# Kernel optimization log

Hardware: AMD Instinct MI355X
Metric: run time of the kernel (lower is better)

## Reference

```python
import math
import jax, jax.numpy as jnp
import numpy as np

B, S, D_MODEL, NUM_HEADS = 4, 2048, 1024, 16
D_N = D_MODEL // NUM_HEADS  # 64


def setup_inputs() -> dict:
    key = jax.random.key(0)
    ks = jax.random.split(key, 10)
    scale = 1.0 / math.sqrt(D_MODEL)
    return {
        "q": jax.random.normal(ks[0], (B, S, D_MODEL), dtype=jnp.float32),
        "k": jax.random.normal(ks[1], (B, S, D_MODEL), dtype=jnp.float32),
        "v": jax.random.normal(ks[2], (B, S, D_MODEL), dtype=jnp.float32),
        "mask": jax.random.uniform(ks[3], (B, S, S), dtype=jnp.float32),
        "w_q": jax.random.normal(ks[4], (D_N, D_MODEL), dtype=jnp.float32) * scale,
        "b_q": jnp.zeros((D_N,), dtype=jnp.float32),
        "w_k": jax.random.normal(ks[5], (D_N, D_MODEL), dtype=jnp.float32) * scale,
        "b_k": jnp.zeros((D_N,), dtype=jnp.float32),
        "w_v": jax.random.normal(ks[6], (D_N, D_MODEL), dtype=jnp.float32) * scale,
        "b_v": jnp.zeros((D_N,), dtype=jnp.float32),
    }


def reference(q, k, v, mask, w_q, b_q, w_k, b_k, w_v, b_v):
    # Linear projections d_model -> d_n (torch Linear: x @ W.T + b)
    qp = jnp.einsum("bsd,nd->bsn", q, w_q) + b_q  # [B,S,d_n]
    kp = jnp.einsum("bsd,nd->bsn", k, w_k) + b_k
    vp = jnp.einsum("bsd,nd->bsn", v, w_v) + b_v
    # Scaled dot-product scores with additive mask penalty
    scores = jnp.einsum("bqn,bkn->bqk", qp, kp) / math.sqrt(D_N) + mask * (-1e9)
    attn = jax.nn.softmax(scores, axis=-1)  # [B,S,S]
    return jnp.einsum("bqk,bkn->bqn", attn, vp)  # [B,S,d_n]
```

## Files before the change

### kernel.cpp

```cpp
#include <hip/hip_runtime.h>
#include <hip/hip_bf16.h>

#define BB 4
#define SS 2048
#define DM 1024
#define DN 64

typedef short short8 __attribute__((ext_vector_type(8)));
typedef float f32x4 __attribute__((ext_vector_type(4)));
typedef unsigned short ushort;

__device__ __forceinline__ ushort f2bf(float f) {
    union { float f; unsigned u; } v; v.f = f;
    unsigned r = v.u + 0x7fffu + ((v.u >> 16) & 1u);
    return (ushort)(r >> 16);
}
__device__ __forceinline__ float bf2f(ushort h) {
    union { unsigned u; float f; } v; v.u = ((unsigned)h) << 16; return v.f;
}

__global__ __launch_bounds__(256) void prep_w(
    const float* __restrict__ wq, const float* __restrict__ wk,
    const float* __restrict__ wv, ushort* __restrict__ w_bf)
{
    int i = blockIdx.x * 256 + threadIdx.x;
    int p = i >> 14;
    int j = (i & 16383) * 4;
    const float* src = (p == 0) ? wq : (p == 1) ? wk : wv;
    float4 f = *(const float4*)(src + j);
    ushort o[4] = { f2bf(f.x), f2bf(f.y), f2bf(f.z), f2bf(f.w) };
    *(unsigned long long*)(w_bf + p * 65536 + j) = *(unsigned long long*)o;
}

__global__ __launch_bounds__(256) void proj_kernel(
    const float* __restrict__ q, const float* __restrict__ k, const float* __restrict__ v,
    const ushort* __restrict__ w_bf,
    const float* __restrict__ bq, const float* __restrict__ bk, const float* __restrict__ bvp,
    ushort* __restrict__ qp, ushort* __restrict__ kp, ushort* __restrict__ vpT)
{
    __shared__ __align__(16) ushort A_lds[2][32][136];

    const int tid  = threadIdx.x;
    const int proj = blockIdx.y;
    const int m0   = blockIdx.x * 32;

    const float* x    = (proj == 0) ? q  : (proj == 1) ? k  : v;
    const ushort* wb  = w_bf + proj * 65536;
    const float* bias = (proj == 0) ? bq : (proj == 1) ? bk : bvp;

    const int wv   = tid >> 6;
    const int lane = tid & 63;
    const int l16  = lane & 15;
    const int quad = lane >> 4;
    const int rg   = wv & 1;
    const int nh   = wv >> 1;

    const int srow = tid >> 5;
    const int slc  = tid & 31;

    float4 pf[4];
    auto issue_loads = [&](int kb) {
#pragma unroll
        for (int r = 0; r < 4; r++)
            pf[r] = *(const float4*)&x[(size_t)(m0 + srow + r * 8) * DM + kb + slc * 4];
    };
    auto write_stage = [&](int buf) {
#pragma unroll
        for (int r = 0; r < 4; r++) {
            ushort t4[4] = { f2bf(pf[r].x), f2bf(pf[r].y), f2bf(pf[r].z), f2bf(pf[r].w) };
            *(unsigned long long*)&A_lds[buf][srow + r * 8][slc * 4] =
                *(unsigned long long*)t4;
        }
    };

    f32x4 acc[2];
    acc[0] = (f32x4){0.f, 0.f, 0.f, 0.f};
    acc[1] = (f32x4){0.f, 0.f, 0.f, 0.f};

    issue_loads(0);

#pragma unroll
    for (int s = 0; s < 8; s++) {
        const int buf = s & 1;
        write_stage(buf);
        if (s < 7) issue_loads((s + 1) * 128);
        __syncthreads();

        const int kb = s * 128;
#pragma unroll
        for (int kk = 0; kk < 128; kk += 32) {
            short8 a = *(const short8*)&A_lds[buf][rg * 16 + l16][kk + quad * 8];
#pragma unroll
            for (int tt = 0; tt < 2; tt++) {
                const int t = nh * 2 + tt;
                short8 b = *(const short8*)(wb + (size_t)(t * 16 + l16) * DM + kb + kk + quad * 8);
                acc[tt] = __builtin_amdgcn_mfma_f32_16x16x32_bf16(a, b, acc[tt], 0, 0, 0);
            }
        }
    }

#pragma unroll
    for (int tt = 0; tt < 2; tt++) {
        const int n = (nh * 2 + tt) * 16 + l16;
        float bb_ = bias[n];
#pragma unroll
        for (int r = 0; r < 4; r++) {
            int grow = m0 + rg * 16 + quad * 4 + r;
            ushort h = f2bf(acc[tt][r] + bb_);
            if (proj == 0)      qp[(size_t)grow * DN + n] = h;
            else if (proj == 1) kp[(size_t)grow * DN + n] = h;
            else {
                int bb = grow >> 11, ss = grow & 2047;
                vpT[((size_t)bb * DN + n) * SS + ss] = h;
            }
        }
    }
}

template<int KPS>
__global__ __launch_bounds__(256, 2) void flash_kernel(
    const float* __restrict__ mask,
    const ushort* __restrict__ qp,
    const ushort* __restrict__ kp,
    const ushort* __restrict__ vpT,
    ushort* __restrict__ part_O,
    float* __restrict__ part_ml)
{
    constexpr int NSLICE = SS / KPS;
    constexpr int NIT    = KPS / 64;

    __shared__ __align__(16) ushort p_lds[4][16][72];

    const int tid  = threadIdx.x;
    const int wv   = tid >> 6;
    const int lane = tid & 63;
    const int l16  = lane & 15;
    const int quad = lane >> 4;

    const int gw    = blockIdx.x * 4 + wv;
    const int qg    = gw & 127;
    const int rest  = gw >> 7;
    const int slice = rest % NSLICE;
    const int b     = rest / NSLICE;

    const ushort* qbase = qp + ((size_t)b * SS + qg * 16 + l16) * DN + quad * 8;
    short8 aq0 = *(const short8*)(qbase);
    short8 aq1 = *(const short8*)(qbase + 32);

    float m_r[4] = { -__builtin_inff(), -__builtin_inff(),
                     -__builtin_inff(), -__builtin_inff() };
    float l_r[4] = { 0.f, 0.f, 0.f, 0.f };
    f32x4 Oacc[4];
#pragma unroll
    for (int t = 0; t < 4; t++) Oacc[t] = (f32x4){0.f, 0.f, 0.f, 0.f};

    const size_t mrow0 = ((size_t)b * SS + qg * 16 + quad * 4) * SS;
    const int k_begin = slice * KPS;

    float  mk[2][4][4];
    short8 bk0[2][4], bk1[2][4];

    auto load_tile = [&](int buf, int k0) {
#pragma unroll
        for (int t = 0; t < 4; t++) {
            const ushort* kb_ = kp + ((size_t)b * SS + k0 + t * 16 + l16) * DN + quad * 8;
            bk0[buf][t] = *(const short8*)(kb_);
            bk1[buf][t] = *(const short8*)(kb_ + 32);
        }
#pragma unroll
        for (int t = 0; t < 4; t++)
#pragma unroll
            for (int r = 0; r < 4; r++)
                mk[buf][t][r] = mask[mrow0 + (size_t)r * SS + k0 + t * 16 + l16];
    };

    load_tile(0, k_begin);

#pragma unroll
    for (int it = 0; it < NIT; ++it) {
        const int cur = it & 1;
        const int k0  = k_begin + it * 64;

        if (it + 1 < NIT) load_tile(cur ^ 1, k0 + 64);

        short8 bv0[4], bv1[4];
#pragma unroll
        for (int tf = 0; tf < 4; tf++) {
            const ushort* vb_ = vpT + ((size_t)b * DN + tf * 16 + l16) * SS + k0 + quad * 8;
            bv0[tf] = *(const short8*)(vb_);
            bv1[tf] = *(const short8*)(vb_ + 32);
        }

        f32x4 sc[4];
#pragma unroll
        for (int t = 0; t < 4; t++) {
            f32x4 z = (f32x4){0.f, 0.f, 0.f, 0.f};
            z = __builtin_amdgcn_mfma_f32_16x16x32_bf16(aq0, bk0[cur][t], z, 0, 0, 0);
            z = __builtin_amdgcn_mfma_f32_16x16x32_bf16(aq1, bk1[cur][t], z, 0, 0, 0);
            sc[t] = z;
        }

#pragma unroll
        for (int r = 0; r < 4; r++) {
            float s[4];
            float tmax = -__builtin_inff();
#pragma unroll
            for (int t = 0; t < 4; t++) {
                s[t] = sc[t][r] * 0.125f - 1e9f * mk[cur][t][r];
                tmax = fmaxf(tmax, s[t]);
            }
#pragma unroll
            for (int off = 8; off >= 1; off >>= 1)
                tmax = fmaxf(tmax, __shfl_xor(tmax, off, 16));
            float mnew  = fmaxf(m_r[r], tmax);
            float alpha = __expf(m_r[r] - mnew);
            m_r[r] = mnew;
            float rs = 0.f;
#pragma unroll
            for (int t = 0; t < 4; t++) {
                float pv = __expf(s[t] - mnew);
                rs += pv;
                p_lds[wv][quad * 4 + r][t * 16 + l16] = f2bf(pv);
            }
#pragma unroll
            for (int off = 8; off >= 1; off >>= 1)
                rs += __shfl_xor(rs, off, 16);
            l_r[r] = l_r[r] * alpha + rs;
#pragma unroll
            for (int tf = 0; tf < 4; tf++)
                Oacc[tf][r] *= alpha;
        }

        short8 ap0 = *(const short8*)&p_lds[wv][l16][quad * 8];
        short8 ap1 = *(const short8*)&p_lds[wv][l16][32 + quad * 8];
#pragma unroll
        for (int tf = 0; tf < 4; tf++) {
            Oacc[tf] = __builtin_amdgcn_mfma_f32_16x16x32_bf16(ap0, bv0[tf], Oacc[tf], 0, 0, 0);
            Oacc[tf] = __builtin_amdgcn_mfma_f32_16x16x32_bf16(ap1, bv1[tf], Oacc[tf], 0, 0, 0);
        }
    }

    const int rowg = (b * SS + qg * 16) + quad * 4;
#pragma unroll
    for (int r = 0; r < 4; r++) {
        size_t row = (size_t)rowg + r;
        if (l16 == 0) {
            part_ml[((size_t)slice * (BB * SS) + row) * 2 + 0] = m_r[r];
            part_ml[((size_t)slice * (BB * SS) + row) * 2 + 1] = l_r[r];
        }
#pragma unroll
        for (int tf = 0; tf < 4; tf++)
            part_O[((size_t)slice * (BB * SS) + row) * DN + tf * 16 + l16] =
                f2bf(Oacc[tf][r]);
    }
}

__global__ __launch_bounds__(256) void combine_kernel(
    const ushort* __restrict__ part_O, const float* __restrict__ part_ml,
    float* __restrict__ out, int nslice)
{
    const int tid = threadIdx.x;
    const int row = blockIdx.x * 4 + (tid >> 6);
    const int f   = tid & 63;

    float ms[8], ls[8];
    float M = -__builtin_inff();
    for (int i = 0; i < nslice; i++) {
        ms[i] = part_ml[((size_t)i * (BB * SS) + row) * 2 + 0];
        ls[i] = part_ml[((size_t)i * (BB * SS) + row) * 2 + 1];
        M = fmaxf(M, ms[i]);
    }
    float L = 0.f, acc = 0.f;
    for (int i = 0; i < nslice; i++) {
        float e = __expf(ms[i] - M);
        L += e * ls[i];
        acc += e * bf2f(part_O[((size_t)i * (BB * SS) + row) * DN + f]);
    }
    out[(size_t)row * DN + f] = acc / L;
}

extern "C" void kernel_launch(void* const* d_in, const int* in_sizes, int n_in,
                              void* d_out, int out_size, void* d_ws, size_t ws_size,
                              hipStream_t stream) {
    const float* q    = (const float*)d_in[0];
    const float* k    = (const float*)d_in[1];
    const float* v    = (const float*)d_in[2];
    const float* mask = (const float*)d_in[3];
    const float* wq   = (const float*)d_in[4];
    const float* bq   = (const float*)d_in[5];
    const float* wk   = (const float*)d_in[6];
    const float* bk   = (const float*)d_in[7];
    const float* wv   = (const float*)d_in[8];
    const float* bv   = (const float*)d_in[9];
    float* out = (float*)d_out;

    char* p = (char*)d_ws;
    ushort* w_bf = (ushort*)p;   p += 3 * 65536 * sizeof(ushort);
    ushort* qp   = (ushort*)p;   p += (size_t)BB * SS * DN * 2;
    ushort* kp   = (ushort*)p;   p += (size_t)BB * SS * DN * 2;
    ushort* vpT  = (ushort*)p;   p += (size_t)BB * SS * DN * 2;
    size_t fixed = (size_t)(p - (char*)d_ws);

    int split = 8;
    for (;;) {
        size_t flash_bytes = (size_t)split * BB * SS * 2 * 4 + (size_t)split * BB * SS * DN * 2;
        if (split == 1 || fixed + flash_bytes <= ws_size) break;
        split >>= 1;
    }

    float*  part_ml = (float*)p;   p += (size_t)split * BB * SS * 2 * 4;
    ushort* part_O  = (ushort*)p;

    prep_w<<<192, 256, 0, stream>>>(wq, wk, wv, w_bf);
    proj_kernel<<<dim3(256, 3), 256, 0, stream>>>(q, k, v, w_bf, bq, bk, bv, qp, kp, vpT);
    switch (split) {
        case 8:  flash_kernel<256> <<<128 * 8, 256, 0, stream>>>(mask, qp, kp, vpT, part_O, part_ml); break;
        case 4:  flash_kernel<512> <<<128 * 4, 256, 0, stream>>>(mask, qp, kp, vpT, part_O, part_ml); break;
        case 2:  flash_kernel<1024><<<128 * 2, 256, 0, stream>>>(mask, qp, kp, vpT, part_O, part_ml); break;
        default: flash_kernel<2048><<<128 * 1, 256, 0, stream>>>(mask, qp, kp, vpT, part_O, part_ml); break;
    }
    combine_kernel<<<(BB * SS) / 4, 256, 0, stream>>>(part_O, part_ml, out, split);
}
```

Measured before the change: 226.9 us.

## Fuse weight conversion into projection, stage weights in LDS, MFMA row sums

Drops the separate prep_w launch. The projection kernel now converts fp32 weights to bf16 itself and stages them in LDS in 256-column chunks, while the activation rows are loaded straight into registers with a four-deep prefetch and converted per step. In the flash kernel the softmax is reorganised to batch the row-max shuffles across the four rows. The row sum is now computed with an extra MFMA against a ones vector instead of shuffle reductions. This removes one launch and the shuffle work, but every block re-reads and re-converts the weights, and the row sum now comes from bf16-rounded probabilities.

```diff
diff --git a/kernel.cpp b/kernel.cpp
--- a/kernel.cpp
+++ b/kernel.cpp
@@ -18,34 +18,26 @@
 __device__ __forceinline__ float bf2f(ushort h) {
     union { unsigned u; float f; } v; v.u = ((unsigned)h) << 16; return v.f;
 }
-
-__global__ __launch_bounds__(256) void prep_w(
-    const float* __restrict__ wq, const float* __restrict__ wk,
-    const float* __restrict__ wv, ushort* __restrict__ w_bf)
-{
-    int i = blockIdx.x * 256 + threadIdx.x;
-    int p = i >> 14;
-    int j = (i & 16383) * 4;
-    const float* src = (p == 0) ? wq : (p == 1) ? wk : wv;
-    float4 f = *(const float4*)(src + j);
-    ushort o[4] = { f2bf(f.x), f2bf(f.y), f2bf(f.z), f2bf(f.w) };
-    *(unsigned long long*)(w_bf + p * 65536 + j) = *(unsigned long long*)o;
-}
-
-__global__ __launch_bounds__(256) void proj_kernel(
+__device__ __forceinline__ short8 cvt8(float4 a, float4 b) {
+    ushort t[8] = { f2bf(a.x), f2bf(a.y), f2bf(a.z), f2bf(a.w),
+                    f2bf(b.x), f2bf(b.y), f2bf(b.z), f2bf(b.w) };
+    return *(short8*)t;
+}
+
+__global__ __launch_bounds__(256, 3) void proj_kernel(
     const float* __restrict__ q, const float* __restrict__ k, const float* __restrict__ v,
-    const ushort* __restrict__ w_bf,
+    const float* __restrict__ wq, const float* __restrict__ wk, const float* __restrict__ wvm,
     const float* __restrict__ bq, const float* __restrict__ bk, const float* __restrict__ bvp,
     ushort* __restrict__ qp, ushort* __restrict__ kp, ushort* __restrict__ vpT)
 {
-    __shared__ __align__(16) ushort A_lds[2][32][136];
+    __shared__ __align__(16) ushort B_lds[64][264];
 
     const int tid  = threadIdx.x;
     const int proj = blockIdx.y;
     const int m0   = blockIdx.x * 32;
 
     const float* x    = (proj == 0) ? q  : (proj == 1) ? k  : v;
-    const ushort* wb  = w_bf + proj * 65536;
+    const float* wm   = (proj == 0) ? wq : (proj == 1) ? wk : wvm;
     const float* bias = (proj == 0) ? bq : (proj == 1) ? bk : bvp;
 
     const int wv   = tid >> 6;
@@ -55,45 +47,44 @@
     const int rg   = wv & 1;
     const int nh   = wv >> 1;
 
-    const int srow = tid >> 5;
-    const int slc  = tid & 31;
-
-    float4 pf[4];
-    auto issue_loads = [&](int kb) {
-#pragma unroll
-        for (int r = 0; r < 4; r++)
-            pf[r] = *(const float4*)&x[(size_t)(m0 + srow + r * 8) * DM + kb + slc * 4];
-    };
-    auto write_stage = [&](int buf) {
-#pragma unroll
-        for (int r = 0; r < 4; r++) {
-            ushort t4[4] = { f2bf(pf[r].x), f2bf(pf[r].y), f2bf(pf[r].z), f2bf(pf[r].w) };
-            *(unsigned long long*)&A_lds[buf][srow + r * 8][slc * 4] =
-                *(unsigned long long*)t4;
-        }
-    };
+    const float* arow = x + (size_t)(m0 + rg * 16 + l16) * DM + quad * 8;
+
+    float4 apf[4][2];
+#pragma unroll
+    for (int s = 0; s < 4; s++) {
+        apf[s][0] = *(const float4*)(arow + s * 32);
+        apf[s][1] = *(const float4*)(arow + s * 32 + 4);
+    }
 
     f32x4 acc[2];
     acc[0] = (f32x4){0.f, 0.f, 0.f, 0.f};
     acc[1] = (f32x4){0.f, 0.f, 0.f, 0.f};
 
-    issue_loads(0);
-
-#pragma unroll
-    for (int s = 0; s < 8; s++) {
-        const int buf = s & 1;
-        write_stage(buf);
-        if (s < 7) issue_loads((s + 1) * 128);
+    for (int c = 0; c < 4; c++) {
         __syncthreads();
-
-        const int kb = s * 128;
-#pragma unroll
-        for (int kk = 0; kk < 128; kk += 32) {
-            short8 a = *(const short8*)&A_lds[buf][rg * 16 + l16][kk + quad * 8];
+#pragma unroll
+        for (int j = 0; j < 16; j++) {
+            int u   = tid + j * 256;
+            int row = u >> 6, c4 = u & 63;
+            float4 f = *(const float4*)(wm + (size_t)row * DM + c * 256 + c4 * 4);
+            ushort t4[4] = { f2bf(f.x), f2bf(f.y), f2bf(f.z), f2bf(f.w) };
+            *(unsigned long long*)&B_lds[row][c4 * 4] = *(unsigned long long*)t4;
+        }
+        __syncthreads();
+
+#pragma unroll
+        for (int kk = 0; kk < 8; kk++) {
+            const int step = c * 8 + kk;
+            const int ai   = step & 3;
+            short8 a = cvt8(apf[ai][0], apf[ai][1]);
+            if (step + 4 < 32) {
+                apf[ai][0] = *(const float4*)(arow + (step + 4) * 32);
+                apf[ai][1] = *(const float4*)(arow + (step + 4) * 32 + 4);
+            }
 #pragma unroll
             for (int tt = 0; tt < 2; tt++) {
                 const int t = nh * 2 + tt;
-                short8 b = *(const short8*)(wb + (size_t)(t * 16 + l16) * DM + kb + kk + quad * 8);
+                short8 b = *(const short8*)&B_lds[t * 16 + l16][kk * 32 + quad * 8];
                 acc[tt] = __builtin_amdgcn_mfma_f32_16x16x32_bf16(a, b, acc[tt], 0, 0, 0);
             }
         }
@@ -147,12 +138,15 @@
     short8 aq0 = *(const short8*)(qbase);
     short8 aq1 = *(const short8*)(qbase + 32);
 
+    ushort onev[8] = { 0x3F80, 0x3F80, 0x3F80, 0x3F80, 0x3F80, 0x3F80, 0x3F80, 0x3F80 };
+    short8 bone = *(short8*)onev;
+
     float m_r[4] = { -__builtin_inff(), -__builtin_inff(),
                      -__builtin_inff(), -__builtin_inff() };
-    float l_r[4] = { 0.f, 0.f, 0.f, 0.f };
-    f32x4 Oacc[4];
+    f32x4 Oacc[4], Lacc;
 #pragma unroll
     for (int t = 0; t < 4; t++) Oacc[t] = (f32x4){0.f, 0.f, 0.f, 0.f};
+    Lacc = (f32x4){0.f, 0.f, 0.f, 0.f};
 
     const size_t mrow0 = ((size_t)b * SS + qg * 16 + quad * 4) * SS;
     const int k_begin = slice * KPS;
@@ -186,9 +180,9 @@
         short8 bv0[4], bv1[4];
 #pragma unroll
         for (int tf = 0; tf < 4; tf++) {
-            const ushort* vb_ = vpT + ((size_t)b * DN + tf * 16 + l16) * SS + k0 + quad * 8;
-            bv0[tf] = *(const short8*)(vb_);
-            bv1[tf] = *(const short8*)(vb_ + 32);
+            const ushort* p_ = vpT + ((size_t)b * DN + tf * 16 + l16) * SS + k0 + quad * 8;
+            bv0[tf] = *(const short8*)p_;
+            bv1[tf] = *(const short8*)(p_ + 32);
         }
 
         f32x4 sc[4];
@@ -200,36 +194,41 @@
             sc[t] = z;
         }
 
+        float s[4][4], tmax[4];
+#pragma unroll
+        for (int r = 0; r < 4; r++) tmax[r] = -__builtin_inff();
+#pragma unroll
+        for (int t = 0; t < 4; t++)
+#pragma unroll
+            for (int r = 0; r < 4; r++) {
+                s[t][r] = sc[t][r] * 0.125f - 1e9f * mk[cur][t][r];
+                tmax[r] = fmaxf(tmax[r], s[t][r]);
+            }
+#pragma unroll
+        for (int off = 8; off >= 1; off >>= 1)
+#pragma unroll
+            for (int r = 0; r < 4; r++)
+                tmax[r] = fmaxf(tmax[r], __shfl_xor(tmax[r], off, 16));
+
+        float alpha[4];
 #pragma unroll
         for (int r = 0; r < 4; r++) {
-            float s[4];
-            float tmax = -__builtin_inff();
-#pragma unroll
-            for (int t = 0; t < 4; t++) {
-                s[t] = sc[t][r] * 0.125f - 1e9f * mk[cur][t][r];
-                tmax = fmaxf(tmax, s[t]);
-            }
-#pragma unroll
-            for (int off = 8; off >= 1; off >>= 1)
-                tmax = fmaxf(tmax, __shfl_xor(tmax, off, 16));
-            float mnew  = fmaxf(m_r[r], tmax);
-            float alpha = __expf(m_r[r] - mnew);
+            float mnew = fmaxf(m_r[r], tmax[r]);
+            alpha[r] = __expf(m_r[r] - mnew);
             m_r[r] = mnew;
-            float rs = 0.f;
-#pragma unroll
-            for (int t = 0; t < 4; t++) {
-                float pv = __expf(s[t] - mnew);
-                rs += pv;
-                p_lds[wv][quad * 4 + r][t * 16 + l16] = f2bf(pv);
-            }
-#pragma unroll
-            for (int off = 8; off >= 1; off >>= 1)
-                rs += __shfl_xor(rs, off, 16);
-            l_r[r] = l_r[r] * alpha + rs;
-#pragma unroll
-            for (int tf = 0; tf < 4; tf++)
-                Oacc[tf][r] *= alpha;
-        }
+        }
+#pragma unroll
+        for (int t = 0; t < 4; t++)
+#pragma unroll
+            for (int r = 0; r < 4; r++)
+                p_lds[wv][quad * 4 + r][t * 16 + l16] = f2bf(__expf(s[t][r] - m_r[r]));
+#pragma unroll
+        for (int tf = 0; tf < 4; tf++)
+#pragma unroll
+            for (int r = 0; r < 4; r++)
+                Oacc[tf][r] *= alpha[r];
+#pragma unroll
+        for (int r = 0; r < 4; r++) Lacc[r] *= alpha[r];
 
         short8 ap0 = *(const short8*)&p_lds[wv][l16][quad * 8];
         short8 ap1 = *(const short8*)&p_lds[wv][l16][32 + quad * 8];
@@ -238,6 +237,8 @@
             Oacc[tf] = __builtin_amdgcn_mfma_f32_16x16x32_bf16(ap0, bv0[tf], Oacc[tf], 0, 0, 0);
             Oacc[tf] = __builtin_amdgcn_mfma_f32_16x16x32_bf16(ap1, bv1[tf], Oacc[tf], 0, 0, 0);
         }
+        Lacc = __builtin_amdgcn_mfma_f32_16x16x32_bf16(ap0, bone, Lacc, 0, 0, 0);
+        Lacc = __builtin_amdgcn_mfma_f32_16x16x32_bf16(ap1, bone, Lacc, 0, 0, 0);
     }
 
     const int rowg = (b * SS + qg * 16) + quad * 4;
@@ -246,7 +247,7 @@
         size_t row = (size_t)rowg + r;
         if (l16 == 0) {
             part_ml[((size_t)slice * (BB * SS) + row) * 2 + 0] = m_r[r];
-            part_ml[((size_t)slice * (BB * SS) + row) * 2 + 1] = l_r[r];
+            part_ml[((size_t)slice * (BB * SS) + row) * 2 + 1] = Lacc[r];
         }
 #pragma unroll
         for (int tf = 0; tf < 4; tf++)
@@ -295,10 +296,9 @@
     float* out = (float*)d_out;
 
     char* p = (char*)d_ws;
-    ushort* w_bf = (ushort*)p;   p += 3 * 65536 * sizeof(ushort);
-    ushort* qp   = (ushort*)p;   p += (size_t)BB * SS * DN * 2;
-    ushort* kp   = (ushort*)p;   p += (size_t)BB * SS * DN * 2;
-    ushort* vpT  = (ushort*)p;   p += (size_t)BB * SS * DN * 2;
+    ushort* qp  = (ushort*)p;   p += (size_t)BB * SS * DN * 2;
+    ushort* kp  = (ushort*)p;   p += (size_t)BB * SS * DN * 2;
+    ushort* vpT = (ushort*)p;   p += (size_t)BB * SS * DN * 2;
     size_t fixed = (size_t)(p - (char*)d_ws);
 
     int split = 8;
@@ -311,8 +311,8 @@
     float*  part_ml = (float*)p;   p += (size_t)split * BB * SS * 2 * 4;
     ushort* part_O  = (ushort*)p;
 
-    prep_w<<<192, 256, 0, stream>>>(wq, wk, wv, w_bf);
-    proj_kernel<<<dim3(256, 3), 256, 0, stream>>>(q, k, v, w_bf, bq, bk, bv, qp, kp, vpT);
+    proj_kernel<<<dim3(256, 3), 256, 0, stream>>>(q, k, v, wq, wk, wv, bq, bk, bv,
+                                                  qp, kp, vpT);
     switch (split) {
         case 8:  flash_kernel<256> <<<128 * 8, 256, 0, stream>>>(mask, qp, kp, vpT, part_O, part_ml); break;
         case 4:  flash_kernel<512> <<<128 * 4, 256, 0, stream>>>(mask, qp, kp, vpT, part_O, part_ml); break;
```

Result: slower. 261.8 us (+15.4%).
